# Kernel tuning notes

Measured on AMD Instinct MI355X. Metric: run time of the kernel, lower is better.

The kernel has to match this reference:

```python
import jax, jax.numpy as jnp
import numpy as np

H = 1024   # HIDDEN_DIM
V = 15000  # VOCAB_SIZE
L = 2      # NUM_LAYERS
E = 4      # experts per block
B, S = 32, 2048


def rmsnorm(x, w, eps=1e-6):
    return x * jax.lax.rsqrt(jnp.mean(x * x, axis=-1, keepdims=True) + eps) * w


def setup_inputs() -> dict:
    key = jax.random.key(0)
    ks = jax.random.split(key, 8)
    windows = jax.random.randint(ks[0], (B, S), 0, V, dtype=jnp.int32)
    hemis = jax.random.randint(ks[1], (B,), 0, 2, dtype=jnp.int32)
    experts = jax.random.randint(ks[2], (B,), 0, E, dtype=jnp.int32)
    emb = jax.random.normal(ks[3], (V, H), dtype=jnp.float32) * 0.02
    norm1_w = jnp.ones((L, H), dtype=jnp.float32)
    decay_logit = jnp.full((L, H), 2.0, dtype=jnp.float32)  # torch init: ones*2.0
    norm2_w = jnp.ones((L, H), dtype=jnp.float32)
    # expert weights, torch Linear layout [out, in] per expert: [L, E, H, H]
    Wexp = jax.random.normal(ks[4], (L, E, H, H), dtype=jnp.float32) * 0.02
    final_norm_w = jnp.ones((H,), dtype=jnp.float32)
    lm_head = jax.random.normal(ks[5], (V, H), dtype=jnp.float32) * 0.02
    return dict(windows=windows, hemis=hemis, experts=experts, emb=emb,
                norm1_w=norm1_w, decay_logit=decay_logit, norm2_w=norm2_w,
                Wexp=Wexp, final_norm_w=final_norm_w, lm_head=lm_head)


def reference(windows, hemis, experts, emb, norm1_w, decay_logit, norm2_w,
              Wexp, final_norm_w, lm_head):
    del hemis  # only used for router loss when targets are given (inference path)
    x = emb[windows]  # [B,S,H]
    onehot = jax.nn.one_hot(experts, E, dtype=x.dtype)  # [B,E]
    for l in range(L):
        xn = rmsnorm(x, norm1_w[l])
        decay = jax.nn.sigmoid(decay_logit[l])  # [H]

        def step(state, xt):
            s = state * decay + xt * (1.0 - decay)
            return s, s

        init = jnp.zeros((x.shape[0], H), dtype=x.dtype)
        _, states = jax.lax.scan(step, init, jnp.swapaxes(xn, 0, 1))  # [S,B,H]
        x = x + jnp.swapaxes(states, 0, 1)
        pool = rmsnorm(x, norm2_w[l])[:, -1, :]  # [B,H]
        # all 4 expert FFNs on the pooled state, then select by expert id
        out_all = jax.nn.relu(jnp.einsum('bh,edh->ebd', pool, Wexp[l]))  # [E,B,H]
        out = jnp.einsum('be,ebh->bh', onehot, out_all)  # [B,H]
        x = x + out[:, None, :]
    final_state = rmsnorm(x[:, -1, :], final_norm_w)
    logits = final_state @ lm_head.T  # [B,V]
    return logits
```

## Files before the change

### kernel.cpp

```cpp
#include <hip/hip_runtime.h>
#include <cstddef>

#define H 1024
#define V 15000
#define NE 4
#define B 32
#define S 2048
#define EPS 1e-6f
#define CH 16
#define T0 128
#define NU 938

__device__ __forceinline__ float wave_sum(float x) {
#pragma unroll
  for (int off = 32; off > 0; off >>= 1) x += __shfl_down(x, off);
  return x;
}

__global__ __launch_bounds__(256) void k_vocab(const float* __restrict__ emb,
                                               float* __restrict__ invr1) {
  const int gw = (blockIdx.x * blockDim.x + threadIdx.x) >> 6;
  const int lane = threadIdx.x & 63;
  if (gw >= V) return;
  const float4* row = (const float4*)(emb + (size_t)gw * H);
  float s = 0.f;
#pragma unroll
  for (int j = 0; j < 4; ++j) {
    const float4 f = row[lane + 64 * j];
    s += f.x * f.x + f.y * f.y + f.z * f.z + f.w * f.w;
  }
  s = wave_sum(s);
  if (lane == 0) invr1[gw] = rsqrtf(s * (1.f / H) + EPS);
}

__global__ __launch_bounds__(1024, 8) void k_scanA(
    const int* __restrict__ windows, const float* __restrict__ emb,
    const float* __restrict__ norm1_w, const float* __restrict__ decay_logit,
    const float* __restrict__ invr1, float* __restrict__ local1) {
  __shared__ int tok_l[T0];
  __shared__ float iv_l[T0];
  const int b = blockIdx.x / CH, c = blockIdx.x % CH;
  const int h = threadIdx.x;
  if (h < T0) {
    const int tok = windows[b * S + c * T0 + h];
    tok_l[h] = tok << 10;
    iv_l[h] = invr1[tok];
  }
  const float d1 = 1.f / (1.f + expf(-decay_logit[h]));
  const float gw = norm1_w[h] * (1.f - d1);
  __syncthreads();
  float s = 0.f;
  for (int t0 = 0; t0 < T0; t0 += 8) {
    float e[8], cv[8];
#pragma unroll
    for (int k = 0; k < 8; ++k) {
      e[k] = emb[(size_t)tok_l[t0 + k] + h];
      cv[k] = iv_l[t0 + k] * gw;
    }
#pragma unroll
    for (int k = 0; k < 8; ++k) s = s * d1 + e[k] * cv[k];
  }
  local1[(size_t)(b * CH + c) * H + h] = s;
}

__global__ __launch_bounds__(1024) void k_scanB(
    const int* __restrict__ windows, const float* __restrict__ emb,
    const float* __restrict__ decay_logit, const float* __restrict__ local1,
    float* __restrict__ s1start, float* __restrict__ es1,
    float* __restrict__ invp) {
  __shared__ float red[16];
  const int b = blockIdx.x, h = threadIdx.x;
  const float d1 = 1.f / (1.f + expf(-decay_logit[h]));
  float dT = d1;
#pragma unroll
  for (int i = 0; i < 7; ++i) dT *= dT;
  float Sv = 0.f;
  for (int c = 0; c < CH; ++c) {
    const size_t idx = (size_t)(b * CH + c) * H + h;
    s1start[idx] = Sv;
    Sv = dT * Sv + local1[idx];
  }
  const int tl = windows[b * S + S - 1];
  const float v = emb[(size_t)tl * H + h] + Sv;
  es1[b * H + h] = v;
  const float q = wave_sum(v * v);
  if ((h & 63) == 0) red[h >> 6] = q;
  __syncthreads();
  if (h == 0) {
    float t = 0.f;
#pragma unroll
    for (int i = 0; i < 16; ++i) t += red[i];
    invp[b] = rsqrtf(t * (1.f / H) + EPS);
  }
}

__global__ __launch_bounds__(256) void k_expert(const float* __restrict__ src,
    const float* __restrict__ invp, const float* __restrict__ n2w,
    const float* __restrict__ Wl, const int* __restrict__ experts,
    float* __restrict__ outp) {
  __shared__ float p[H];
  const int b = blockIdx.x >> 4;
  const int dblk = blockIdx.x & 15;
  const int tid = threadIdx.x;
  const float ip = invp[b];
  for (int j = tid; j < H; j += 256) p[j] = src[b * H + j] * ip * n2w[j];
  __syncthreads();
  const float* W = Wl + (size_t)experts[b] * H * H;
  const int wave = tid >> 6, lane = tid & 63;
#pragma unroll 1
  for (int i = 0; i < 16; ++i) {
    const int dd = dblk * 64 + wave * 16 + i;
    const float* wr = W + (size_t)dd * H;
    float s = 0.f;
#pragma unroll
    for (int j = 0; j < 16; ++j) s += wr[lane + 64 * j] * p[lane + 64 * j];
    s = wave_sum(s);
    if (lane == 0) outp[b * H + dd] = fmaxf(s, 0.f);
  }
}

__global__ __launch_bounds__(1024, 8) void k_sumsqC(
    const int* __restrict__ windows, const float* __restrict__ emb,
    const float* __restrict__ norm1_w, const float* __restrict__ decay_logit,
    const float* __restrict__ invr1, const float* __restrict__ s1start,
    const float* __restrict__ out1, float* __restrict__ r2) {
  __shared__ int tok_l[T0];
  __shared__ float iv_l[T0];
  __shared__ float q[16 * H];
  const int b = blockIdx.x / CH, c = blockIdx.x % CH;
  const int h = threadIdx.x;
  if (h < T0) {
    const int tok = windows[b * S + c * T0 + h];
    tok_l[h] = tok << 10;
    iv_l[h] = invr1[tok];
  }
  const float d1 = 1.f / (1.f + expf(-decay_logit[h]));
  const float gw = norm1_w[h] * (1.f - d1);
  const float o1 = out1[b * H + h];
  float s1 = s1start[(size_t)(b * CH + c) * H + h];
  __syncthreads();
  const int wv = h >> 6, lane = h & 63;
  for (int sb = 0; sb < T0 / 16; ++sb) {
#pragma unroll
    for (int g = 0; g < 2; ++g) {
      float e[8], cv[8];
#pragma unroll
      for (int k = 0; k < 8; ++k) {
        const int t = sb * 16 + g * 8 + k;
        e[k] = emb[(size_t)tok_l[t] + h];
        cv[k] = iv_l[t] * gw;
      }
#pragma unroll
      for (int k = 0; k < 8; ++k) {
        s1 = s1 * d1 + e[k] * cv[k];
        const float x1 = e[k] + s1 + o1;
        q[(g * 8 + k) * H + h] = x1 * x1;
      }
    }
    __syncthreads();
    const float4* q4 = (const float4*)(q + wv * H);
    float ssum = 0.f;
#pragma unroll
    for (int j = 0; j < 4; ++j) {
      const float4 f = q4[lane + 64 * j];
      ssum += f.x + f.y + f.z + f.w;
    }
    ssum = wave_sum(ssum);
    if (lane == 0) r2[b * S + c * T0 + sb * 16 + wv] = ssum;
    __syncthreads();
  }
}

__global__ __launch_bounds__(256) void k_r2fin(float* __restrict__ r2) {
  const int i = blockIdx.x * 256 + threadIdx.x;
  r2[i] = rsqrtf(r2[i] * (1.f / H) + EPS);
}

__global__ __launch_bounds__(1024, 8) void k_scanD(
    const int* __restrict__ windows, const float* __restrict__ emb,
    const float* __restrict__ norm1_w, const float* __restrict__ decay_logit,
    const float* __restrict__ invr1, const float* __restrict__ s1start,
    const float* __restrict__ out1, const float* __restrict__ r2inv,
    float* __restrict__ local2, float* __restrict__ x1last) {
  __shared__ int tok_l[T0];
  __shared__ float iv_l[T0];
  __shared__ float rv_l[T0];
  const int b = blockIdx.x / CH, c = blockIdx.x % CH;
  const int h = threadIdx.x;
  if (h < T0) {
    const int tok = windows[b * S + c * T0 + h];
    tok_l[h] = tok << 10;
    iv_l[h] = invr1[tok];
    rv_l[h] = r2inv[b * S + c * T0 + h];
  }
  const float d1 = 1.f / (1.f + expf(-decay_logit[h]));
  const float g1 = norm1_w[h] * (1.f - d1);
  const float d2 = 1.f / (1.f + expf(-decay_logit[H + h]));
  const float g2 = norm1_w[H + h] * (1.f - d2);
  const float o1 = out1[b * H + h];
  float s1 = s1start[(size_t)(b * CH + c) * H + h];
  __syncthreads();
  float s2 = 0.f, x1 = 0.f;
  for (int t0 = 0; t0 < T0; t0 += 8) {
    float e[8], cv[8], rc[8];
#pragma unroll
    for (int k = 0; k < 8; ++k) {
      e[k] = emb[(size_t)tok_l[t0 + k] + h];
      cv[k] = iv_l[t0 + k] * g1;
      rc[k] = rv_l[t0 + k] * g2;
    }
#pragma unroll
    for (int k = 0; k < 8; ++k) {
      s1 = s1 * d1 + e[k] * cv[k];
      x1 = e[k] + s1 + o1;
      s2 = s2 * d2 + x1 * rc[k];
    }
  }
  local2[(size_t)(b * CH + c) * H + h] = s2;
  if (c == CH - 1) x1last[b * H + h] = x1;
}

__global__ __launch_bounds__(1024) void k_scanE(
    const float* __restrict__ decay_logit, const float* __restrict__ local2,
    const float* __restrict__ x1last, float* __restrict__ es2,
    float* __restrict__ invp) {
  __shared__ float red[16];
  const int b = blockIdx.x, h = threadIdx.x;
  const float d2 = 1.f / (1.f + expf(-decay_logit[H + h]));
  float dT = d2;
#pragma unroll
  for (int i = 0; i < 7; ++i) dT *= dT;
  float Sv = 0.f;
  for (int c = 0; c < CH; ++c)
    Sv = dT * Sv + local2[(size_t)(b * CH + c) * H + h];
  const float v = x1last[b * H + h] + Sv;
  es2[b * H + h] = v;
  const float q = wave_sum(v * v);
  if ((h & 63) == 0) red[h >> 6] = q;
  __syncthreads();
  if (h == 0) {
    float t = 0.f;
#pragma unroll
    for (int i = 0; i < 16; ++i) t += red[i];
    invp[32 + b] = rsqrtf(t * (1.f / H) + EPS);
  }
}

__global__ __launch_bounds__(256) void k_fstate(const float* __restrict__ es2,
    const float* __restrict__ out2, const float* __restrict__ fnw,
    float* __restrict__ fst) {
  __shared__ float red[4];
  const int b = blockIdx.x, tid = threadIdx.x;
  float4 x = ((const float4*)(es2 + b * H))[tid];
  const float4 y = ((const float4*)(out2 + b * H))[tid];
  x.x += y.x; x.y += y.y; x.z += y.z; x.w += y.w;
  float s = x.x * x.x + x.y * x.y + x.z * x.z + x.w * x.w;
  s = wave_sum(s);
  if ((tid & 63) == 0) red[tid >> 6] = s;
  __syncthreads();
  const float ir =
      rsqrtf((red[0] + red[1] + red[2] + red[3]) * (1.f / H) + EPS);
  const float4 w = ((const float4*)fnw)[tid];
  float4 o;
  o.x = x.x * ir * w.x; o.y = x.y * ir * w.y;
  o.z = x.z * ir * w.z; o.w = x.w * ir * w.w;
  ((float4*)(fst + b * H))[tid] = o;
}

__global__ __launch_bounds__(256) void k_logits(const float* __restrict__ fst,
    const float* __restrict__ lm, float* __restrict__ part) {
  __shared__ float4 fs4[16 * 128];
  const int hh = blockIdx.x & 1;
  const int bgrp = (blockIdx.x >> 1) & 1;
  const int vblk = blockIdx.x >> 2;
  const int tid = threadIdx.x;
  for (int j = tid; j < 16 * 128; j += 256) {
    const int bb = j >> 7, q = j & 127;
    fs4[j] = ((const float4*)fst)[(bgrp * 16 + bb) * 256 + hh * 128 + q];
  }
  __syncthreads();
  const int wave = tid >> 6, lane = tid & 63;
  const int sg = lane >> 4;
  const int c = lane & 15;
  const int u = vblk * 4 + wave;
  if (u >= NU) return;
  const int v0 = u * 16 + sg * 4;
  const float4* rp[4];
#pragma unroll
  for (int i = 0; i < 4; ++i) {
    int r = v0 + i;
    if (r > V - 1) r = V - 1;
    rp[i] = (const float4*)(lm + (size_t)r * H) + hh * 128;
  }
  float acc[4][16];
#pragma unroll
  for (int i = 0; i < 4; ++i)
#pragma unroll
    for (int bb = 0; bb < 16; ++bb) acc[i][bb] = 0.f;
  float4 lv[4], lvn[4];
#pragma unroll
  for (int i = 0; i < 4; ++i) lv[i] = rp[i][c];
#pragma unroll 1
  for (int jj = 0; jj < 8; ++jj) {
    const int hoff = c + 16 * jj;
    if (jj < 7) {
#pragma unroll
      for (int i = 0; i < 4; ++i) lvn[i] = rp[i][hoff + 16];
    }
#pragma unroll
    for (int bb = 0; bb < 16; ++bb) {
      const float4 fv = fs4[bb * 128 + hoff];
#pragma unroll
      for (int i = 0; i < 4; ++i) {
        acc[i][bb] += lv[i].x * fv.x + lv[i].y * fv.y + lv[i].z * fv.z +
                      lv[i].w * fv.w;
      }
    }
#pragma unroll
    for (int i = 0; i < 4; ++i) lv[i] = lvn[i];
  }
#pragma unroll
  for (int off = 1; off < 16; off <<= 1)
#pragma unroll
    for (int i = 0; i < 4; ++i)
#pragma unroll
      for (int bb = 0; bb < 16; ++bb)
        acc[i][bb] += __shfl_xor(acc[i][bb], off);
  if (c == 0) {
    float* pdst = part + (size_t)hh * B * V + (size_t)bgrp * 16 * V;
#pragma unroll
    for (int bb = 0; bb < 16; ++bb)
#pragma unroll
      for (int i = 0; i < 4; ++i) {
        const int r = v0 + i;
        if (r < V) pdst[(size_t)bb * V + r] = acc[i][bb];
      }
  }
}

__global__ __launch_bounds__(256) void k_comb(const float* __restrict__ part,
                                              float* __restrict__ outp) {
  const int i = blockIdx.x * 256 + threadIdx.x;
  if (i < B * V) outp[i] = part[i] + part[B * V + i];
}

extern "C" void kernel_launch(void* const* d_in, const int* in_sizes, int n_in,
                              void* d_out, int out_size, void* d_ws,
                              size_t ws_size, hipStream_t stream) {
  const int* windows = (const int*)d_in[0];
  const int* experts = (const int*)d_in[2];
  const float* emb = (const float*)d_in[3];
  const float* norm1_w = (const float*)d_in[4];
  const float* decay_logit = (const float*)d_in[5];
  const float* norm2_w = (const float*)d_in[6];
  const float* Wexp = (const float*)d_in[7];
  const float* final_norm_w = (const float*)d_in[8];
  const float* lm_head = (const float*)d_in[9];
  float* outp = (float*)d_out;

  float* ws = (float*)d_ws;
  float* invr1 = ws;
  float* local1 = invr1 + 15360;
  float* s1start = local1 + B * CH * H;
  float* local2 = s1start + B * CH * H;
  float* out1 = local2 + B * CH * H;
  float* out2 = out1 + B * H;
  float* es1 = out2 + B * H;
  float* es2 = es1 + B * H;
  float* x1last = es2 + B * H;
  float* fst = x1last + B * H;
  float* invp = fst + B * H;
  float* r2 = invp + 64;
  float* part = local1;

  k_vocab<<<(V * 64 + 255) / 256, 256, 0, stream>>>(emb, invr1);
  k_scanA<<<B * CH, 1024, 0, stream>>>(windows, emb, norm1_w, decay_logit,
                                       invr1, local1);
  k_scanB<<<B, 1024, 0, stream>>>(windows, emb, decay_logit, local1, s1start,
                                  es1, invp);
  k_expert<<<B * 16, 256, 0, stream>>>(es1, invp, norm2_w, Wexp, experts,
                                       out1);
  k_sumsqC<<<B * CH, 1024, 0, stream>>>(windows, emb, norm1_w, decay_logit,
                                        invr1, s1start, out1, r2);
  k_r2fin<<<(B * S) / 256, 256, 0, stream>>>(r2);
  k_scanD<<<B * CH, 1024, 0, stream>>>(windows, emb, norm1_w, decay_logit,
                                       invr1, s1start, out1, r2, local2,
                                       x1last);
  k_scanE<<<B, 1024, 0, stream>>>(decay_logit, local2, x1last, es2, invp);
  k_expert<<<B * 16, 256, 0, stream>>>(es2, invp + 32, norm2_w + H,
                                       Wexp + (size_t)NE * H * H, experts,
                                       out2);
  k_fstate<<<B, 256, 0, stream>>>(es2, out2, final_norm_w, fst);
  k_logits<<<940, 256, 0, stream>>>(fst, lm_head, part);
  k_comb<<<(B * V + 255) / 256, 256, 0, stream>>>(part, outp);
}
```

Measured before the change: 354.4 us.

## Bucket batches by expert and fuse layer-2 sumsq and scan kernels

Adds a bucketing kernel that groups batch rows by expert id. The expert FFN then loads each weight row once and reuses it across all batches assigned to that expert, rather than re-reading expert weights per batch. It also fuses the layer-1 recomputation, the per-token RMS computation and the layer-2 local scan into one kernel. That removes a second embedding gather pass and the r2 global round trip, at the cost of extra shared-memory traffic and syncs inside the scan loop. The bucketing kernel runs serially on one thread, and expert load imbalance can leave some blocks idle.

```diff
diff --git a/kernel.cpp b/kernel.cpp
--- a/kernel.cpp
+++ b/kernel.cpp
@@ -31,6 +31,19 @@
   }
   s = wave_sum(s);
   if (lane == 0) invr1[gw] = rsqrtf(s * (1.f / H) + EPS);
+}
+
+__global__ void k_bucket(const int* __restrict__ experts,
+                         int* __restrict__ elist, int* __restrict__ ecnt) {
+  if (threadIdx.x == 0 && blockIdx.x == 0) {
+    int c[NE] = {0, 0, 0, 0};
+    for (int b = 0; b < B; ++b) {
+      const int e = experts[b];
+      elist[e * B + c[e]] = b;
+      c[e]++;
+    }
+    for (int e = 0; e < NE; ++e) ecnt[e] = c[e];
+  }
 }
 
 __global__ __launch_bounds__(1024, 8) void k_scanA(
@@ -94,39 +107,53 @@
   }
 }
 
-__global__ __launch_bounds__(256) void k_expert(const float* __restrict__ src,
-    const float* __restrict__ invp, const float* __restrict__ n2w,
-    const float* __restrict__ Wl, const int* __restrict__ experts,
+__global__ __launch_bounds__(256) void k_expert2(
+    const float* __restrict__ src, const float* __restrict__ invp,
+    const float* __restrict__ n2w, const float* __restrict__ Wl,
+    const int* __restrict__ elist, const int* __restrict__ ecnt,
     float* __restrict__ outp) {
-  __shared__ float p[H];
-  const int b = blockIdx.x >> 4;
-  const int dblk = blockIdx.x & 15;
-  const int tid = threadIdx.x;
-  const float ip = invp[b];
-  for (int j = tid; j < H; j += 256) p[j] = src[b * H + j] * ip * n2w[j];
-  __syncthreads();
-  const float* W = Wl + (size_t)experts[b] * H * H;
-  const int wave = tid >> 6, lane = tid & 63;
+  const int e = blockIdx.x >> 6;
+  const int dgrp = blockIdx.x & 63;
+  const int cnt = ecnt[e];
+  if (cnt == 0) return;
+  const int wave = threadIdx.x >> 6, lane = threadIdx.x & 63;
+  const float* W = Wl + (size_t)e * H * H;
+  const float4* n2w4 = (const float4*)n2w;
 #pragma unroll 1
-  for (int i = 0; i < 16; ++i) {
-    const int dd = dblk * 64 + wave * 16 + i;
-    const float* wr = W + (size_t)dd * H;
-    float s = 0.f;
-#pragma unroll
-    for (int j = 0; j < 16; ++j) s += wr[lane + 64 * j] * p[lane + 64 * j];
-    s = wave_sum(s);
-    if (lane == 0) outp[b * H + dd] = fmaxf(s, 0.f);
-  }
-}
-
-__global__ __launch_bounds__(1024, 8) void k_sumsqC(
+  for (int i = 0; i < 4; ++i) {
+    const int dd = dgrp * 16 + wave * 4 + i;
+    const float4* wr4 = (const float4*)(W + (size_t)dd * H);
+    float4 w4[4];
+#pragma unroll
+    for (int j = 0; j < 4; ++j) w4[j] = wr4[lane + 64 * j];
+#pragma unroll 1
+    for (int bi = 0; bi < cnt; ++bi) {
+      const int b = elist[e * B + bi];
+      const float4* s4 = (const float4*)(src + b * H);
+      float s = 0.f;
+#pragma unroll
+      for (int j = 0; j < 4; ++j) {
+        const float4 sv = s4[lane + 64 * j];
+        const float4 nv = n2w4[lane + 64 * j];
+        s += w4[j].x * sv.x * nv.x + w4[j].y * sv.y * nv.y +
+             w4[j].z * sv.z * nv.z + w4[j].w * sv.w * nv.w;
+      }
+      s = wave_sum(s);
+      if (lane == 0) outp[b * H + dd] = fmaxf(s * invp[b], 0.f);
+    }
+  }
+}
+
+__global__ __launch_bounds__(1024, 8) void k_fuseCD(
     const int* __restrict__ windows, const float* __restrict__ emb,
     const float* __restrict__ norm1_w, const float* __restrict__ decay_logit,
     const float* __restrict__ invr1, const float* __restrict__ s1start,
-    const float* __restrict__ out1, float* __restrict__ r2) {
+    const float* __restrict__ out1, float* __restrict__ local2,
+    float* __restrict__ x1last) {
   __shared__ int tok_l[T0];
   __shared__ float iv_l[T0];
   __shared__ float q[16 * H];
+  __shared__ float rinv_l[16];
   const int b = blockIdx.x / CH, c = blockIdx.x % CH;
   const int h = threadIdx.x;
   if (h < T0) {
@@ -135,89 +162,56 @@
     iv_l[h] = invr1[tok];
   }
   const float d1 = 1.f / (1.f + expf(-decay_logit[h]));
-  const float gw = norm1_w[h] * (1.f - d1);
-  const float o1 = out1[b * H + h];
-  float s1 = s1start[(size_t)(b * CH + c) * H + h];
-  __syncthreads();
-  const int wv = h >> 6, lane = h & 63;
-  for (int sb = 0; sb < T0 / 16; ++sb) {
-#pragma unroll
-    for (int g = 0; g < 2; ++g) {
-      float e[8], cv[8];
-#pragma unroll
-      for (int k = 0; k < 8; ++k) {
-        const int t = sb * 16 + g * 8 + k;
-        e[k] = emb[(size_t)tok_l[t] + h];
-        cv[k] = iv_l[t] * gw;
-      }
-#pragma unroll
-      for (int k = 0; k < 8; ++k) {
-        s1 = s1 * d1 + e[k] * cv[k];
-        const float x1 = e[k] + s1 + o1;
-        q[(g * 8 + k) * H + h] = x1 * x1;
-      }
-    }
-    __syncthreads();
-    const float4* q4 = (const float4*)(q + wv * H);
-    float ssum = 0.f;
-#pragma unroll
-    for (int j = 0; j < 4; ++j) {
-      const float4 f = q4[lane + 64 * j];
-      ssum += f.x + f.y + f.z + f.w;
-    }
-    ssum = wave_sum(ssum);
-    if (lane == 0) r2[b * S + c * T0 + sb * 16 + wv] = ssum;
-    __syncthreads();
-  }
-}
-
-__global__ __launch_bounds__(256) void k_r2fin(float* __restrict__ r2) {
-  const int i = blockIdx.x * 256 + threadIdx.x;
-  r2[i] = rsqrtf(r2[i] * (1.f / H) + EPS);
-}
-
-__global__ __launch_bounds__(1024, 8) void k_scanD(
-    const int* __restrict__ windows, const float* __restrict__ emb,
-    const float* __restrict__ norm1_w, const float* __restrict__ decay_logit,
-    const float* __restrict__ invr1, const float* __restrict__ s1start,
-    const float* __restrict__ out1, const float* __restrict__ r2inv,
-    float* __restrict__ local2, float* __restrict__ x1last) {
-  __shared__ int tok_l[T0];
-  __shared__ float iv_l[T0];
-  __shared__ float rv_l[T0];
-  const int b = blockIdx.x / CH, c = blockIdx.x % CH;
-  const int h = threadIdx.x;
-  if (h < T0) {
-    const int tok = windows[b * S + c * T0 + h];
-    tok_l[h] = tok << 10;
-    iv_l[h] = invr1[tok];
-    rv_l[h] = r2inv[b * S + c * T0 + h];
-  }
-  const float d1 = 1.f / (1.f + expf(-decay_logit[h]));
   const float g1 = norm1_w[h] * (1.f - d1);
   const float d2 = 1.f / (1.f + expf(-decay_logit[H + h]));
   const float g2 = norm1_w[H + h] * (1.f - d2);
   const float o1 = out1[b * H + h];
   float s1 = s1start[(size_t)(b * CH + c) * H + h];
   __syncthreads();
-  float s2 = 0.f, x1 = 0.f;
-  for (int t0 = 0; t0 < T0; t0 += 8) {
-    float e[8], cv[8], rc[8];
-#pragma unroll
-    for (int k = 0; k < 8; ++k) {
-      e[k] = emb[(size_t)tok_l[t0 + k] + h];
-      cv[k] = iv_l[t0 + k] * g1;
-      rc[k] = rv_l[t0 + k] * g2;
-    }
-#pragma unroll
-    for (int k = 0; k < 8; ++k) {
-      s1 = s1 * d1 + e[k] * cv[k];
-      x1 = e[k] + s1 + o1;
-      s2 = s2 * d2 + x1 * rc[k];
-    }
+  const int wv = h >> 6, lane = h & 63;
+  float s2 = 0.f;
+  for (int sb = 0; sb < T0 / 16; ++sb) {
+#pragma unroll
+    for (int g = 0; g < 2; ++g) {
+      float e[8], cv[8];
+#pragma unroll
+      for (int k = 0; k < 8; ++k) {
+        const int t = sb * 16 + g * 8 + k;
+        e[k] = emb[(size_t)tok_l[t] + h];
+        cv[k] = iv_l[t] * g1;
+      }
+#pragma unroll
+      for (int k = 0; k < 8; ++k) {
+        s1 = s1 * d1 + e[k] * cv[k];
+        q[(g * 8 + k) * H + h] = e[k] + s1 + o1;
+      }
+    }
+    __syncthreads();
+    const float4* q4 = (const float4*)(q + wv * H);
+    float ssum = 0.f;
+#pragma unroll
+    for (int j = 0; j < 4; ++j) {
+      const float4 f = q4[lane + 64 * j];
+      ssum += f.x * f.x + f.y * f.y + f.z * f.z + f.w * f.w;
+    }
+    ssum = wave_sum(ssum);
+    if (lane == 0) rinv_l[wv] = rsqrtf(ssum * (1.f / H) + EPS);
+    __syncthreads();
+#pragma unroll
+    for (int g = 0; g < 2; ++g) {
+      float xv[8], rc[8];
+#pragma unroll
+      for (int k = 0; k < 8; ++k) {
+        xv[k] = q[(g * 8 + k) * H + h];
+        rc[k] = rinv_l[g * 8 + k] * g2;
+      }
+#pragma unroll
+      for (int k = 0; k < 8; ++k) s2 = s2 * d2 + xv[k] * rc[k];
+    }
+    __syncthreads();
   }
   local2[(size_t)(b * CH + c) * H + h] = s2;
-  if (c == CH - 1) x1last[b * H + h] = x1;
+  if (c == CH - 1) x1last[b * H + h] = q[15 * H + h];
 }
 
 __global__ __launch_bounds__(1024) void k_scanE(
@@ -370,26 +364,24 @@
   float* x1last = es2 + B * H;
   float* fst = x1last + B * H;
   float* invp = fst + B * H;
-  float* r2 = invp + 64;
+  int* elist = (int*)(invp + 64);
+  int* ecnt = elist + NE * B;
   float* part = local1;
 
   k_vocab<<<(V * 64 + 255) / 256, 256, 0, stream>>>(emb, invr1);
+  k_bucket<<<1, 64, 0, stream>>>(experts, elist, ecnt);
   k_scanA<<<B * CH, 1024, 0, stream>>>(windows, emb, norm1_w, decay_logit,
                                        invr1, local1);
   k_scanB<<<B, 1024, 0, stream>>>(windows, emb, decay_logit, local1, s1start,
                                   es1, invp);
-  k_expert<<<B * 16, 256, 0, stream>>>(es1, invp, norm2_w, Wexp, experts,
-                                       out1);
-  k_sumsqC<<<B * CH, 1024, 0, stream>>>(windows, emb, norm1_w, decay_logit,
-                                        invr1, s1start, out1, r2);
-  k_r2fin<<<(B * S) / 256, 256, 0, stream>>>(r2);
-  k_scanD<<<B * CH, 1024, 0, stream>>>(windows, emb, norm1_w, decay_logit,
-                                       invr1, s1start, out1, r2, local2,
-                                       x1last);
+  k_expert2<<<NE * 64, 256, 0, stream>>>(es1, invp, norm2_w, Wexp, elist,
+                                         ecnt, out1);
+  k_fuseCD<<<B * CH, 1024, 0, stream>>>(windows, emb, norm1_w, decay_logit,
+                                        invr1, s1start, out1, local2, x1last);
   k_scanE<<<B, 1024, 0, stream>>>(decay_logit, local2, x1last, es2, invp);
-  k_expert<<<B * 16, 256, 0, stream>>>(es2, invp + 32, norm2_w + H,
-                                       Wexp + (size_t)NE * H * H, experts,
-                                       out2);
+  k_expert2<<<NE * 64, 256, 0, stream>>>(es2, invp + 32, norm2_w + H,
+                                         Wexp + (size_t)NE * H * H, elist,
+                                         ecnt, out2);
   k_fstate<<<B, 256, 0, stream>>>(es2, out2, final_norm_w, fst);
   k_logits<<<940, 256, 0, stream>>>(fst, lm_head, part);
   k_comb<<<(B * V + 255) / 256, 256, 0, stream>>>(part, outp);
```

After: 334.8 us. 5.5% less time.
